# Kernel optimization log

Measured on AMD Instinct MI355X. Metric: run time of the kernel, lower is better.

Reference implementation:

```python
import jax, jax.numpy as jnp
import numpy as np

B, FP, ENC, H, V, SEQ = 512, 4096, 64, 512, 42, 128


def _lin(k, out_d, in_d, scale=0.05):
    kw, kb = jax.random.split(k)
    return (jax.random.normal(kw, (out_d, in_d), jnp.float32) * scale,
            jax.random.normal(kb, (out_d,), jnp.float32) * scale)


def setup_inputs() -> dict:
    key = jax.random.key(0)
    ks = jax.random.split(key, 16)
    inp = {}
    inp["X"] = jax.random.normal(ks[0], (B, FP), jnp.float32)
    inp["y"] = jax.random.normal(ks[1], (B, SEQ, V), jnp.float32)
    inp["eps"] = jax.random.normal(ks[2], (B, ENC), jnp.float32)
    inp["e_fc1w"], inp["e_fc1b"] = _lin(ks[3], 2048, FP, 0.02)
    inp["e_fc2w"], inp["e_fc2b"] = _lin(ks[4], 1024, 2048)
    inp["e_fc3w"], inp["e_fc3b"] = _lin(ks[5], 512, 1024)
    inp["e_fc41w"], inp["e_fc41b"] = _lin(ks[6], ENC, 512)
    inp["e_fc42w"], inp["e_fc42b"] = _lin(ks[7], ENC, 512)
    inp["d_fc1w"], inp["d_fc1b"] = _lin(ks[8], H, ENC)
    inp["d_fc2w"], inp["d_fc2b"] = _lin(ks[9], V, H)
    inp["w_ih0"], inp["b_ih0"] = _lin(ks[10], 3 * H, V)
    inp["w_hh0"], inp["b_hh0"] = _lin(ks[11], 3 * H, H)
    inp["w_ih1"], inp["b_ih1"] = _lin(ks[12], 3 * H, H)
    inp["w_hh1"], inp["b_hh1"] = _lin(ks[13], 3 * H, H)
    return inp


def _gru_cell(x, h, w_ih, w_hh, b_ih, b_hh):
    # PyTorch GRU gate math.
    gi = x @ w_ih.T + b_ih  # [B, 3H]
    gh = h @ w_hh.T + b_hh  # [B, 3H]
    ir, iz, i_n = jnp.split(gi, 3, axis=-1)
    hr, hz, h_n = jnp.split(gh, 3, axis=-1)
    r = jax.nn.sigmoid(ir + hr)
    z = jax.nn.sigmoid(iz + hz)
    n = jnp.tanh(i_n + r * h_n)
    return (1.0 - z) * n + z * h


def reference(X, y, eps, e_fc1w, e_fc1b, e_fc2w, e_fc2b, e_fc3w, e_fc3b,
              e_fc41w, e_fc41b, e_fc42w, e_fc42b, d_fc1w, d_fc1b,
              d_fc2w, d_fc2b, w_ih0, b_ih0, w_hh0, b_hh0,
              w_ih1, b_ih1, w_hh1, b_hh1):
    # --- VAE encoder ---
    h1 = jax.nn.relu(X @ e_fc1w.T + e_fc1b)
    h2 = jax.nn.relu(h1 @ e_fc2w.T + e_fc2b)
    h3 = jax.nn.relu(h2 @ e_fc3w.T + e_fc3b)
    mu = h3 @ e_fc41w.T + e_fc41b
    logvar = h3 @ e_fc42w.T + e_fc42b
    kld = jnp.mean(-0.5 * jnp.sum(1.0 + logvar - mu ** 2 - jnp.exp(logvar), axis=1))
    encoded = eps * jnp.exp(0.5 * logvar) + mu  # reparameterize (eps supplied)

    batch = X.shape[0]
    lat = encoded @ d_fc1w.T + d_fc1b  # [B, H]
    hid0 = jnp.zeros((2, batch, H), X.dtype).at[0].set(lat)
    start = jnp.zeros((V,), X.dtype).at[41].set(1.0)
    x0 = jnp.broadcast_to(start, (batch, V))

    def step(carry, _):
        x, hid = carry
        h_l0 = _gru_cell(x, hid[0], w_ih0, w_hh0, b_ih0, b_hh0)
        h_l1 = _gru_cell(h_l0, hid[1], w_ih1, w_hh1, b_ih1, b_hh1)
        out = h_l1 @ d_fc2w.T + d_fc2b  # [B, V]
        return (out, jnp.stack([h_l0, h_l1])), out

    _, outs = jax.lax.scan(step, (x0, hid0), None, length=SEQ)
    decoded = jnp.transpose(outs, (1, 0, 2))  # [B, SEQ, V]
    return decoded, kld
```

## Files before the change

kernel.cpp:

```cpp
#include <hip/hip_runtime.h>
#include <math.h>

constexpr int kB = 512, kENC = 64, kH = 512, kV = 42, kSEQ = 128;
constexpr int kWPitch = 520;
constexpr int kWRows  = 96;
constexpr int kZPad   = kWRows * kWPitch;
constexpr int kCsAByte = (kZPad + 32) * 2;
constexpr int kLdsBytes = kCsAByte + 30720 + 15360 + 480;

typedef __attribute__((ext_vector_type(8))) short bf16x8;
typedef __attribute__((ext_vector_type(4))) float f32x4;
typedef unsigned long long u64;

__device__ __forceinline__ unsigned short f2bf(float x) {
  union { float f; unsigned u; } c; c.f = x;
  unsigned r = c.u + 0x7FFFu + ((c.u >> 16) & 1u);
  return (unsigned short)(r >> 16);
}
__device__ __forceinline__ float sigm(float x) { return 1.f / (1.f + expf(-x)); }

__device__ __forceinline__ void ld_row16(const unsigned short* p, bf16x8 (&r)[16]) {
  asm volatile(
    "global_load_dwordx4 %0, %16, off sc0 sc1\n\t"
    "global_load_dwordx4 %1, %16, off offset:64 sc0 sc1\n\t"
    "global_load_dwordx4 %2, %16, off offset:128 sc0 sc1\n\t"
    "global_load_dwordx4 %3, %16, off offset:192 sc0 sc1\n\t"
    "global_load_dwordx4 %4, %16, off offset:256 sc0 sc1\n\t"
    "global_load_dwordx4 %5, %16, off offset:320 sc0 sc1\n\t"
    "global_load_dwordx4 %6, %16, off offset:384 sc0 sc1\n\t"
    "global_load_dwordx4 %7, %16, off offset:448 sc0 sc1\n\t"
    "global_load_dwordx4 %8, %16, off offset:512 sc0 sc1\n\t"
    "global_load_dwordx4 %9, %16, off offset:576 sc0 sc1\n\t"
    "global_load_dwordx4 %10, %16, off offset:640 sc0 sc1\n\t"
    "global_load_dwordx4 %11, %16, off offset:704 sc0 sc1\n\t"
    "global_load_dwordx4 %12, %16, off offset:768 sc0 sc1\n\t"
    "global_load_dwordx4 %13, %16, off offset:832 sc0 sc1\n\t"
    "global_load_dwordx4 %14, %16, off offset:896 sc0 sc1\n\t"
    "global_load_dwordx4 %15, %16, off offset:960 sc0 sc1\n\t"
    "s_waitcnt vmcnt(0)"
    : "=&v"(r[0]), "=&v"(r[1]), "=&v"(r[2]), "=&v"(r[3]),
      "=&v"(r[4]), "=&v"(r[5]), "=&v"(r[6]), "=&v"(r[7]),
      "=&v"(r[8]), "=&v"(r[9]), "=&v"(r[10]), "=&v"(r[11]),
      "=&v"(r[12]), "=&v"(r[13]), "=&v"(r[14]), "=&v"(r[15])
    : "v"(p)
    : "memory");
}

__device__ __forceinline__ void st_h2(unsigned short* p, unsigned short v) {
  __hip_atomic_store(p, v, __ATOMIC_RELAXED, __HIP_MEMORY_SCOPE_AGENT);
}

__device__ __forceinline__ void mg_barrier(unsigned* bar, unsigned ev, int mg,
                                           int jg, int wave, int lane) {
  __syncthreads();
  if (wave == 0) {
    if (lane == 0)
      __hip_atomic_store(&bar[(mg * 64 + jg) * 16], ev,
                         __ATOMIC_RELEASE, __HIP_MEMORY_SCOPE_AGENT);
    const unsigned* sl = &bar[(mg * 64 + lane) * 16];
    while (__hip_atomic_load(sl, __ATOMIC_RELAXED, __HIP_MEMORY_SCOPE_AGENT) < ev)
      __builtin_amdgcn_s_sleep(1);
    (void)__hip_atomic_load(sl, __ATOMIC_ACQUIRE, __HIP_MEMORY_SCOPE_AGENT);
  }
  __syncthreads();
}

template<bool RELU>
__global__ __launch_bounds__(256) void gemm_bias(const float* __restrict__ A,
    const float* __restrict__ W, const float* __restrict__ bias,
    float* __restrict__ C, int M, int N, int K)
{
  __shared__ float As[16][68];
  __shared__ float Bs[16][68];
  const int tid = threadIdx.x;
  const int n0 = blockIdx.x * 64;
  const int m0 = blockIdx.y * 64;
  const int tx = tid & 15;
  const int ty = tid >> 4;
  const int lr = tid >> 2;
  const int lk = (tid & 3) << 2;
  float acc[4][4] = {};
  for (int kc = 0; kc < K; kc += 16) {
    const float4 va = *(const float4*)(A + (size_t)(m0 + lr) * K + kc + lk);
    const float4 vb = *(const float4*)(W + (size_t)(n0 + lr) * K + kc + lk);
    __syncthreads();
    As[lk+0][lr] = va.x; As[lk+1][lr] = va.y; As[lk+2][lr] = va.z; As[lk+3][lr] = va.w;
    Bs[lk+0][lr] = vb.x; Bs[lk+1][lr] = vb.y; Bs[lk+2][lr] = vb.z; Bs[lk+3][lr] = vb.w;
    __syncthreads();
#pragma unroll
    for (int k = 0; k < 16; ++k) {
      const float4 a = *(const float4*)&As[k][ty << 2];
      const float4 b = *(const float4*)&Bs[k][tx << 2];
      const float av[4] = {a.x, a.y, a.z, a.w};
      const float bv[4] = {b.x, b.y, b.z, b.w};
#pragma unroll
      for (int i = 0; i < 4; ++i)
#pragma unroll
        for (int jj = 0; jj < 4; ++jj) acc[i][jj] = fmaf(av[i], bv[jj], acc[i][jj]);
    }
  }
  const int cn = n0 + (tx << 2);
  const float4 b4 = *(const float4*)&bias[cn];
  const float bvv[4] = {b4.x, b4.y, b4.z, b4.w};
#pragma unroll
  for (int i = 0; i < 4; ++i) {
    float4 o;
    float* op = &o.x;
#pragma unroll
    for (int jj = 0; jj < 4; ++jj) {
      float v = acc[i][jj] + bvv[jj];
      if (RELU) v = fmaxf(v, 0.f);
      op[jj] = v;
    }
    *(float4*)(C + (size_t)(m0 + (ty << 2) + i) * N + cn) = o;
  }
}

__global__ __launch_bounds__(256) void enc_kld(const float* __restrict__ mu,
    const float* __restrict__ lv, const float* __restrict__ eps,
    float* __restrict__ enc, float* __restrict__ kld)
{
  const int idx = blockIdx.x * 256 + threadIdx.x;
  const float m = mu[idx], l = lv[idx];
  enc[idx] = eps[idx] * expf(0.5f * l) + m;
  float term = 1.0f + l - m * m - expf(l);
  __shared__ float red[256];
  red[threadIdx.x] = term;
  __syncthreads();
  for (int s = 128; s > 0; s >>= 1) {
    if (threadIdx.x < s) red[threadIdx.x] += red[threadIdx.x + s];
    __syncthreads();
  }
  if (threadIdx.x == 0) atomicAdd(kld, -0.5f * red[0] / (float)kB);
}

__global__ __launch_bounds__(256) void prep_comb(const float* __restrict__ wih0,
    const float* __restrict__ bih0, const float* __restrict__ fc2w,
    const float* __restrict__ fc2b, unsigned short* __restrict__ Wcb,
    float* __restrict__ bc, float* __restrict__ g0)
{
  const int idx = blockIdx.x * 256 + threadIdx.x;
  const int n = idx >> 9, j = idx & 511;
  float s = 0.f;
#pragma unroll
  for (int v = 0; v < kV; ++v) s = fmaf(wih0[n * kV + v], fc2w[v * kH + j], s);
  Wcb[idx] = f2bf(s);
  if (j == 0) {
    float sb = 0.f;
    for (int v = 0; v < kV; ++v) sb = fmaf(wih0[n * kV + v], fc2b[v], sb);
    bc[n] = bih0[n] + sb;
  }
  if (j == 1) g0[n] = wih0[n * kV + 41] + bih0[n];
}

__global__ __launch_bounds__(256) void conv_bf16(const float* __restrict__ s,
                                                 unsigned short* __restrict__ d, int n)
{
  const int i = blockIdx.x * 256 + threadIdx.x;
  if (i < n) d[i] = f2bf(s[i]);
}

__global__ __launch_bounds__(256) void conv_fc2w_pad(const float* __restrict__ fc2w,
                                                     unsigned short* __restrict__ d)
{
  const int i = blockIdx.x * 256 + threadIdx.x;
  if (i < 48 * kH) {
    const int r = i >> 9, k = i & 511;
    d[i] = (r < kV) ? f2bf(fc2w[r * kH + k]) : 0;
  }
}

__global__ __launch_bounds__(1024) void gru_mfma(
    const unsigned short* __restrict__ Wcb, const unsigned short* __restrict__ whh0b,
    const unsigned short* __restrict__ wih1b, const unsigned short* __restrict__ whh1b,
    const unsigned short* __restrict__ fc2wb,
    const float* __restrict__ bc, const float* __restrict__ g0,
    const float* __restrict__ bhh0, const float* __restrict__ bih1,
    const float* __restrict__ bhh1, const float* __restrict__ fc2b,
    const float* __restrict__ latg,
    unsigned short* h0A, unsigned short* h0B,
    unsigned short* h1A, unsigned short* h1B,
    float* __restrict__ out, unsigned* bar)
{
  extern __shared__ char smem[];
  unsigned short* w = (unsigned short*)smem;
  float* CsA = (float*)(smem + kCsAByte);
  float* CsB = CsA + 7680;
  float* bt  = CsB + 3840;

  const int tid = threadIdx.x;
  const int wave = tid >> 6;
  const int lane = tid & 63;
  const int quad = lane >> 4;
  const int flr  = lane & 15;
  const int q8   = quad * 8;
  const int bid = blockIdx.x;
  const int jg = bid >> 2, mg = bid & 3;
  const int jbase = jg * 8;
  const int m0 = mg * 128;

  for (int c = tid; c < kWRows * 64; c += 1024) {
    const int row = c >> 6;
    const int k8 = (c & 63) << 3;
    const unsigned short* src;
    int srow;
    if (row < 48) {
      const int g = row >> 4, n = row & 15;
      srow = g * kH + jbase + (n & 7);
      src = (n < 8) ? Wcb : whh1b;
    } else if (row < 72) {
      const int rr = row - 48;
      srow = (rr >> 3) * kH + jbase + (rr & 7);
      src = whh0b;
    } else {
      const int rr = row - 72;
      srow = (rr >> 3) * kH + jbase + (rr & 7);
      src = wih1b;
    }
    *(uint4*)&w[row * kWPitch + k8] = *(const uint4*)&src[(size_t)srow * kH + k8];
  }
  if (tid < 32) w[kZPad + tid] = 0;

  if (tid < 120) {
    const int r = tid >> 3, jjl = tid & 7;
    const int jj = jbase + jjl;
    float v;
    if (r < 3)       v = g0[r * kH + jj];
    else if (r < 6)  v = bc[(r - 3) * kH + jj];
    else if (r < 9)  v = bhh0[(r - 6) * kH + jj];
    else if (r < 12) v = bih1[(r - 9) * kH + jj];
    else             v = bhh1[(r - 12) * kH + jj];
    bt[tid] = v;
  }

  int boffT0[3], boffT1[3], boffB[3];
#pragma unroll
  for (int g = 0; g < 3; ++g) {
    boffT0[g] = (g * 16 + flr) * kWPitch + q8;
    boffT1[g] = (flr < 8) ? (48 + g * 8 + flr) * kWPitch + q8 : kZPad + q8;
    boffB[g]  = (flr < 8) ? (72 + g * 8 + flr) * kWPitch + q8 : kZPad + q8;
  }

  const int gm = tid >> 3;
  const int jl = tid & 7;
  const int gmt = gm >> 4, gml = gm & 15;
  const int j = jbase + jl;

  float hp0 = latg[(size_t)(m0 + gm) * kH + j];
  float hp1 = 0.f;

  const bool isProj = (jg < 3) && (wave >= 8);
  const int pv = jg * 16 + flr;
  const float fbv = (isProj && pv < kV) ? fc2b[pv] : 0.f;

  __syncthreads();

  const unsigned short* h0c = h0A; unsigned short* h0n_ = h0B;
  const unsigned short* h1c = h1A; unsigned short* h1n_ = h1B;
  const f32x4 zf = {0.f, 0.f, 0.f, 0.f};

  bf16x8 ar[16];
  if (wave < 8) {
    const unsigned short* ap0 = h0c + (size_t)(m0 + wave * 16 + flr) * kH + q8;
    ld_row16(ap0, ar);
  }

  for (int t = 0; t < kSEQ; ++t) {
    if (wave >= 8) {
      const int wv = wave - 8;
      const unsigned short* ap = h1c + (size_t)(m0 + wv * 16 + flr) * kH + q8;
      ld_row16(ap, ar);
      f32x4 acc[3] = {zf, zf, zf};
#pragma unroll
      for (int kf = 0; kf < 16; ++kf) {
        const int ko = kf * 32;
#pragma unroll
        for (int g = 0; g < 3; ++g)
          acc[g] = __builtin_amdgcn_mfma_f32_16x16x32_bf16(
              ar[kf], *(const bf16x8*)&w[boffT0[g] + ko], acc[g], 0, 0, 0);
      }
#pragma unroll
      for (int g = 0; g < 3; ++g)
        *(f32x4*)&CsA[((g * 8 + wv) * 16 + flr) * 20 + quad * 4] = acc[g];
    } else {
      f32x4 acc[3] = {zf, zf, zf};
#pragma unroll
      for (int kf = 0; kf < 16; ++kf) {
        const int ko = kf * 32;
#pragma unroll
        for (int g = 0; g < 3; ++g)
          acc[g] = __builtin_amdgcn_mfma_f32_16x16x32_bf16(
              ar[kf], *(const bf16x8*)&w[boffT1[g] + ko], acc[g], 0, 0, 0);
      }
      if (flr < 8) {
#pragma unroll
        for (int g = 0; g < 3; ++g)
          *(f32x4*)&CsB[((g * 8 + wave) * 8 + flr) * 20 + quad * 4] = acc[g];
      }
    }
    __syncthreads();
    {
      const float gir = CsA[((0 * 8 + gmt) * 16 + jl) * 20 + gml] + bt[(t == 0 ? 0 : 3) * 8 + jl];
      const float giz = CsA[((1 * 8 + gmt) * 16 + jl) * 20 + gml] + bt[(t == 0 ? 1 : 4) * 8 + jl];
      const float gin = CsA[((2 * 8 + gmt) * 16 + jl) * 20 + gml] + bt[(t == 0 ? 2 : 5) * 8 + jl];
      const float ghr = CsB[((0 * 8 + gmt) * 8 + jl) * 20 + gml] + bt[6 * 8 + jl];
      const float ghz = CsB[((1 * 8 + gmt) * 8 + jl) * 20 + gml] + bt[7 * 8 + jl];
      const float ghn = CsB[((2 * 8 + gmt) * 8 + jl) * 20 + gml] + bt[8 * 8 + jl];
      const float r = sigm(gir + ghr);
      const float z = sigm(giz + ghz);
      const float n = tanhf(gin + r * ghn);
      const float h = (1.f - z) * n + z * hp0;
      hp0 = h;
      st_h2(h0n_ + (size_t)(m0 + gm) * kH + j, f2bf(h));
    }
    mg_barrier(bar, (unsigned)(2 * t + 1), mg, jg, wave, lane);
    if (wave < 8) {
      const unsigned short* ap = h0n_ + (size_t)(m0 + wave * 16 + flr) * kH + q8;
      ld_row16(ap, ar);
      f32x4 acc[3] = {zf, zf, zf};
#pragma unroll
      for (int kf = 0; kf < 16; ++kf) {
        const int ko = kf * 32;
#pragma unroll
        for (int g = 0; g < 3; ++g)
          acc[g] = __builtin_amdgcn_mfma_f32_16x16x32_bf16(
              ar[kf], *(const bf16x8*)&w[boffB[g] + ko], acc[g], 0, 0, 0);
      }
      if (flr < 8) {
#pragma unroll
        for (int g = 0; g < 3; ++g)
          *(f32x4*)&CsB[((g * 8 + wave) * 8 + flr) * 20 + quad * 4] = acc[g];
      }
    } else if (isProj && t > 0) {
      const int mt = wave - 8;
      const unsigned short* bp = fc2wb + (size_t)(jg * 16 + flr) * kH + q8;
      f32x4 pa = zf;
#pragma unroll
      for (int kf = 0; kf < 16; ++kf) {
        const int ko = kf * 32;
        pa = __builtin_amdgcn_mfma_f32_16x16x32_bf16(
            ar[kf], *(const bf16x8*)(bp + ko), pa, 0, 0, 0);
      }
      if (pv < kV) {
#pragma unroll
        for (int r = 0; r < 4; ++r)
          out[(size_t)(m0 + mt * 16 + quad * 4 + r) * (kSEQ * kV)
              + (size_t)(t - 1) * kV + pv] = pa[r] + fbv;
      }
    }
    __syncthreads();
    {
      const float gir = CsB[((0 * 8 + gmt) * 8 + jl) * 20 + gml] + bt[9 * 8 + jl];
      const float giz = CsB[((1 * 8 + gmt) * 8 + jl) * 20 + gml] + bt[10 * 8 + jl];
      const float gin = CsB[((2 * 8 + gmt) * 8 + jl) * 20 + gml] + bt[11 * 8 + jl];
      const float ghr = CsA[((0 * 8 + gmt) * 16 + 8 + jl) * 20 + gml] + bt[12 * 8 + jl];
      const float ghz = CsA[((1 * 8 + gmt) * 16 + 8 + jl) * 20 + gml] + bt[13 * 8 + jl];
      const float ghn = CsA[((2 * 8 + gmt) * 16 + 8 + jl) * 20 + gml] + bt[14 * 8 + jl];
      const float r = sigm(gir + ghr);
      const float z = sigm(giz + ghz);
      const float n = tanhf(gin + r * ghn);
      const float h = (1.f - z) * n + z * hp1;
      hp1 = h;
      st_h2(h1n_ + (size_t)(m0 + gm) * kH + j, f2bf(h));
    }
    mg_barrier(bar, (unsigned)(2 * t + 2), mg, jg, wave, lane);
    {
      const unsigned short* tc;
      tc = h0c; h0c = h0n_; h0n_ = (unsigned short*)tc;
      tc = h1c; h1c = h1n_; h1n_ = (unsigned short*)tc;
    }
  }
  if (isProj) {
    const int mt = wave - 8;
    const unsigned short* ap = h1c + (size_t)(m0 + mt * 16 + flr) * kH + q8;
    const unsigned short* bp = fc2wb + (size_t)(jg * 16 + flr) * kH + q8;
    ld_row16(ap, ar);
    f32x4 pa = zf;
#pragma unroll
    for (int kf = 0; kf < 16; ++kf) {
      const int ko = kf * 32;
      pa = __builtin_amdgcn_mfma_f32_16x16x32_bf16(
          ar[kf], *(const bf16x8*)(bp + ko), pa, 0, 0, 0);
    }
    if (pv < kV) {
#pragma unroll
      for (int r = 0; r < 4; ++r)
        out[(size_t)(m0 + mt * 16 + quad * 4 + r) * (kSEQ * kV)
            + (size_t)(kSEQ - 1) * kV + pv] = pa[r] + fbv;
    }
  }
}

extern "C" void kernel_launch(void* const* d_in, const int* in_sizes, int n_in,
                              void* d_out, int out_size, void* d_ws, size_t ws_size,
                              hipStream_t stream) {
  const float* X    = (const float*)d_in[0];
  const float* eps  = (const float*)d_in[2];
  const float* e1w  = (const float*)d_in[3];  const float* e1b  = (const float*)d_in[4];
  const float* e2w  = (const float*)d_in[5];  const float* e2b  = (const float*)d_in[6];
  const float* e3w  = (const float*)d_in[7];  const float* e3b  = (const float*)d_in[8];
  const float* e41w = (const float*)d_in[9];  const float* e41b = (const float*)d_in[10];
  const float* e42w = (const float*)d_in[11]; const float* e42b = (const float*)d_in[12];
  const float* fc1w = (const float*)d_in[13]; const float* fc1b = (const float*)d_in[14];
  const float* fc2w = (const float*)d_in[15]; const float* fc2b = (const float*)d_in[16];
  const float* wih0 = (const float*)d_in[17]; const float* bih0 = (const float*)d_in[18];
  const float* whh0 = (const float*)d_in[19]; const float* bhh0 = (const float*)d_in[20];
  const float* wih1 = (const float*)d_in[21]; const float* bih1 = (const float*)d_in[22];
  const float* whh1 = (const float*)d_in[23]; const float* bhh1 = (const float*)d_in[24];
  float* out = (float*)d_out;

  float* ws = (float*)d_ws;
  float* eh1 = ws;
  unsigned short* Wcb   = (unsigned short*)(ws + 0);
  unsigned short* whh0b = (unsigned short*)(ws + 393216);
  unsigned short* fc2wb = (unsigned short*)(ws + 786432);
  float* eh2 = ws + 1048576;
  unsigned short* wih1b = (unsigned short*)(ws + 1048576);
  unsigned short* whh1b = (unsigned short*)(ws + 1441792);
  float* eh3 = ws + 1572864;
  float* latg = ws + 1835008;
  unsigned short* h0a = (unsigned short*)(ws + 2097152);
  unsigned short* h0b = (unsigned short*)(ws + 2228224);
  unsigned short* h1a = (unsigned short*)(ws + 2359296);
  unsigned short* h1b = (unsigned short*)(ws + 2490368);
  float* mu  = ws + 2621440;
  float* lv  = ws + 2654208;
  float* enc = ws + 2686976;
  float* bc  = ws + 2719744;
  float* g0  = ws + 2721280;
  unsigned* bar = (unsigned*)(ws + 2723840);

  const size_t dec_elems = (size_t)kB * kSEQ * kV;

  gemm_bias<true ><<<dim3(32, 8), 256, 0, stream>>>(X,   e1w, e1b, eh1, kB, 2048, 4096);
  gemm_bias<true ><<<dim3(16, 8), 256, 0, stream>>>(eh1, e2w, e2b, eh2, kB, 1024, 2048);
  gemm_bias<true ><<<dim3( 8, 8), 256, 0, stream>>>(eh2, e3w, e3b, eh3, kB,  512, 1024);
  gemm_bias<false><<<dim3( 1, 8), 256, 0, stream>>>(eh3, e41w, e41b, mu, kB,   64,  512);
  gemm_bias<false><<<dim3( 1, 8), 256, 0, stream>>>(eh3, e42w, e42b, lv, kB,   64,  512);
  hipMemsetAsync(out + dec_elems, 0, sizeof(float), stream);
  enc_kld<<<128, 256, 0, stream>>>(mu, lv, eps, enc, out + dec_elems);
  gemm_bias<false><<<dim3(8, 8), 256, 0, stream>>>(enc, fc1w, fc1b, latg, kB, kH, kENC);

  prep_comb<<<3072, 256, 0, stream>>>(wih0, bih0, fc2w, fc2b, Wcb, bc, g0);
  conv_bf16<<<3072, 256, 0, stream>>>(whh0, whh0b, 1536 * kH);
  conv_bf16<<<3072, 256, 0, stream>>>(wih1, wih1b, 1536 * kH);
  conv_bf16<<<3072, 256, 0, stream>>>(whh1, whh1b, 1536 * kH);
  conv_fc2w_pad<<<96, 256, 0, stream>>>(fc2w, fc2wb);
  conv_bf16<<<1024, 256, 0, stream>>>(latg, h0a, kB * kH);
  hipMemsetAsync(h1a, 0, (size_t)kB * kH * sizeof(unsigned short), stream);
  hipMemsetAsync(bar, 0, 16384, stream);

  hipFuncSetAttribute((const void*)gru_mfma,
                      hipFuncAttributeMaxDynamicSharedMemorySize, kLdsBytes);
  void* args[] = { (void*)&Wcb, (void*)&whh0b, (void*)&wih1b, (void*)&whh1b,
                   (void*)&fc2wb, (void*)&bc, (void*)&g0, (void*)&bhh0,
                   (void*)&bih1, (void*)&bhh1, (void*)&fc2b, (void*)&latg,
                   (void*)&h0a, (void*)&h0b, (void*)&h1a, (void*)&h1b,
                   (void*)&out, (void*)&bar };
  hipLaunchCooperativeKernel((void*)gru_mfma, dim3(256), dim3(1024), args,
                             kLdsBytes, stream);
}
```

Baseline: 3.527 ms.

## Replace per-group barrier with global barrier and relax load cache bypass

The per-batch-group barrier, where one wave spun on 64 flags, becomes a grid-wide barrier. Up to 256 threads each poll one block's flag, followed by a single agent-scope acquire fence. The hidden-state row loads drop the sc1 bit and keep only sc0, and the output projection stores become relaxed agent-scope atomic stores. The goal is cheaper state loads that can hit in a closer cache level, at the cost of every block waiting on all blocks at each half-step instead of only its own group.

```diff
diff --git a/kernel.cpp b/kernel.cpp
--- a/kernel.cpp
+++ b/kernel.cpp
@@ -21,22 +21,22 @@
 
 __device__ __forceinline__ void ld_row16(const unsigned short* p, bf16x8 (&r)[16]) {
   asm volatile(
-    "global_load_dwordx4 %0, %16, off sc0 sc1\n\t"
-    "global_load_dwordx4 %1, %16, off offset:64 sc0 sc1\n\t"
-    "global_load_dwordx4 %2, %16, off offset:128 sc0 sc1\n\t"
-    "global_load_dwordx4 %3, %16, off offset:192 sc0 sc1\n\t"
-    "global_load_dwordx4 %4, %16, off offset:256 sc0 sc1\n\t"
-    "global_load_dwordx4 %5, %16, off offset:320 sc0 sc1\n\t"
-    "global_load_dwordx4 %6, %16, off offset:384 sc0 sc1\n\t"
-    "global_load_dwordx4 %7, %16, off offset:448 sc0 sc1\n\t"
-    "global_load_dwordx4 %8, %16, off offset:512 sc0 sc1\n\t"
-    "global_load_dwordx4 %9, %16, off offset:576 sc0 sc1\n\t"
-    "global_load_dwordx4 %10, %16, off offset:640 sc0 sc1\n\t"
-    "global_load_dwordx4 %11, %16, off offset:704 sc0 sc1\n\t"
-    "global_load_dwordx4 %12, %16, off offset:768 sc0 sc1\n\t"
-    "global_load_dwordx4 %13, %16, off offset:832 sc0 sc1\n\t"
-    "global_load_dwordx4 %14, %16, off offset:896 sc0 sc1\n\t"
-    "global_load_dwordx4 %15, %16, off offset:960 sc0 sc1\n\t"
+    "global_load_dwordx4 %0, %16, off sc0\n\t"
+    "global_load_dwordx4 %1, %16, off offset:64 sc0\n\t"
+    "global_load_dwordx4 %2, %16, off offset:128 sc0\n\t"
+    "global_load_dwordx4 %3, %16, off offset:192 sc0\n\t"
+    "global_load_dwordx4 %4, %16, off offset:256 sc0\n\t"
+    "global_load_dwordx4 %5, %16, off offset:320 sc0\n\t"
+    "global_load_dwordx4 %6, %16, off offset:384 sc0\n\t"
+    "global_load_dwordx4 %7, %16, off offset:448 sc0\n\t"
+    "global_load_dwordx4 %8, %16, off offset:512 sc0\n\t"
+    "global_load_dwordx4 %9, %16, off offset:576 sc0\n\t"
+    "global_load_dwordx4 %10, %16, off offset:640 sc0\n\t"
+    "global_load_dwordx4 %11, %16, off offset:704 sc0\n\t"
+    "global_load_dwordx4 %12, %16, off offset:768 sc0\n\t"
+    "global_load_dwordx4 %13, %16, off offset:832 sc0\n\t"
+    "global_load_dwordx4 %14, %16, off offset:896 sc0\n\t"
+    "global_load_dwordx4 %15, %16, off offset:960 sc0\n\t"
     "s_waitcnt vmcnt(0)"
     : "=&v"(r[0]), "=&v"(r[1]), "=&v"(r[2]), "=&v"(r[3]),
       "=&v"(r[4]), "=&v"(r[5]), "=&v"(r[6]), "=&v"(r[7]),
@@ -49,19 +49,23 @@
 __device__ __forceinline__ void st_h2(unsigned short* p, unsigned short v) {
   __hip_atomic_store(p, v, __ATOMIC_RELAXED, __HIP_MEMORY_SCOPE_AGENT);
 }
-
-__device__ __forceinline__ void mg_barrier(unsigned* bar, unsigned ev, int mg,
-                                           int jg, int wave, int lane) {
+__device__ __forceinline__ void st_f32(float* p, float v) {
+  __hip_atomic_store(p, v, __ATOMIC_RELAXED, __HIP_MEMORY_SCOPE_AGENT);
+}
+
+__device__ __forceinline__ void g_barrier(unsigned* bar, unsigned ev, int bid, int tid) {
   __syncthreads();
-  if (wave == 0) {
-    if (lane == 0)
-      __hip_atomic_store(&bar[(mg * 64 + jg) * 16], ev,
-                         __ATOMIC_RELEASE, __HIP_MEMORY_SCOPE_AGENT);
-    const unsigned* sl = &bar[(mg * 64 + lane) * 16];
+  if (tid == 0)
+    __hip_atomic_store(&bar[bid * 16], ev,
+                       __ATOMIC_RELEASE, __HIP_MEMORY_SCOPE_AGENT);
+  if (tid < 256) {
+    const unsigned* sl = &bar[tid * 16];
     while (__hip_atomic_load(sl, __ATOMIC_RELAXED, __HIP_MEMORY_SCOPE_AGENT) < ev)
       __builtin_amdgcn_s_sleep(1);
-    (void)__hip_atomic_load(sl, __ATOMIC_ACQUIRE, __HIP_MEMORY_SCOPE_AGENT);
-  }
+  }
+  __syncthreads();
+  if (tid == 0)
+    __builtin_amdgcn_fence(__ATOMIC_ACQUIRE, "agent");
   __syncthreads();
 }
 
@@ -313,7 +317,7 @@
       hp0 = h;
       st_h2(h0n_ + (size_t)(m0 + gm) * kH + j, f2bf(h));
     }
-    mg_barrier(bar, (unsigned)(2 * t + 1), mg, jg, wave, lane);
+    g_barrier(bar, (unsigned)(2 * t + 1), bid, tid);
     if (wave < 8) {
       const unsigned short* ap = h0n_ + (size_t)(m0 + wave * 16 + flr) * kH + q8;
       ld_row16(ap, ar);
@@ -344,8 +348,8 @@
       if (pv < kV) {
 #pragma unroll
         for (int r = 0; r < 4; ++r)
-          out[(size_t)(m0 + mt * 16 + quad * 4 + r) * (kSEQ * kV)
-              + (size_t)(t - 1) * kV + pv] = pa[r] + fbv;
+          st_f32(&out[(size_t)(m0 + mt * 16 + quad * 4 + r) * (kSEQ * kV)
+                      + (size_t)(t - 1) * kV + pv], pa[r] + fbv);
       }
     }
     __syncthreads();
@@ -363,7 +367,7 @@
       hp1 = h;
       st_h2(h1n_ + (size_t)(m0 + gm) * kH + j, f2bf(h));
     }
-    mg_barrier(bar, (unsigned)(2 * t + 2), mg, jg, wave, lane);
+    g_barrier(bar, (unsigned)(2 * t + 2), bid, tid);
     {
       const unsigned short* tc;
       tc = h0c; h0c = h0n_; h0n_ = (unsigned short*)tc;
@@ -385,8 +389,8 @@
     if (pv < kV) {
 #pragma unroll
       for (int r = 0; r < 4; ++r)
-        out[(size_t)(m0 + mt * 16 + quad * 4 + r) * (kSEQ * kV)
-            + (size_t)(kSEQ - 1) * kV + pv] = pa[r] + fbv;
+        st_f32(&out[(size_t)(m0 + mt * 16 + quad * 4 + r) * (kSEQ * kV)
+                    + (size_t)(kSEQ - 1) * kV + pv], pa[r] + fbv);
     }
   }
 }
```

Result: slower. 3.789 ms (+7.4%).
